# Performance work log

Measured on AMD Instinct MI355X. Metric: run time of the kernel, lower is better.

## Reference

```python
import jax, jax.numpy as jnp
import numpy as np

DIM = 1024; HEADS = 16; DHEAD = 64; HID = 2048; E = 8; TOPK = 2
B = 2; S = 1024; SCTX = 1024
SCALE = DHEAD ** -0.5
INNER = HEADS * DHEAD


def setup_inputs() -> dict:
    key = jax.random.key(0)
    ks = jax.random.split(key, 20)
    w = lambda k, shape: jax.random.normal(k, shape, dtype=jnp.float32) * 0.02
    return {
        'x': jax.random.normal(ks[0], (B, S, DIM), dtype=jnp.float32),
        'enc_output': jax.random.normal(ks[1], (B, SCTX, DIM), dtype=jnp.float32),
        'src_mask': jnp.zeros((B, SCTX), dtype=bool),
        'tgt_mask': jax.random.randint(ks[2], (B, S), 0, 2).astype(bool),
        'tgt_mask_id_bool': jax.random.randint(ks[3], (B, S), 0, 2).astype(bool),
        'ln1_g': jnp.ones((DIM,), jnp.float32), 'ln1_b': jnp.zeros((DIM,), jnp.float32),
        'ln2_g': jnp.ones((DIM,), jnp.float32), 'ln2_b': jnp.zeros((DIM,), jnp.float32),
        'ln3_g': jnp.ones((DIM,), jnp.float32), 'ln3_b': jnp.zeros((DIM,), jnp.float32),
        'sa_wq': w(ks[4], (DIM, INNER)), 'sa_wk': w(ks[5], (DIM, INNER)),
        'sa_wv': w(ks[6], (DIM, INNER)), 'sa_wo': w(ks[7], (INNER, DIM)),
        'sa_bo': jnp.zeros((DIM,), jnp.float32),
        'ca_wq': w(ks[8], (DIM, INNER)), 'ca_wk': w(ks[9], (DIM, INNER)),
        'ca_wv': w(ks[10], (DIM, INNER)), 'ca_wo': w(ks[11], (INNER, DIM)),
        'ca_bo': jnp.zeros((DIM,), jnp.float32),
        'gate_w': w(ks[12], (DIM, E)),
        'cls_w': w(ks[13], (DIM, 1)), 'cls_b': jnp.zeros((1,), jnp.float32),
        'moe_w1': w(ks[14], (E, DIM, HID)),
        'moe_w2': w(ks[15], (E, HID, DIM)),
        'moe_w3': w(ks[16], (E, DIM, HID)),
    }


def layer_norm(x, g, b, eps=1e-5):
    m = jnp.mean(x, -1, keepdims=True)
    v = jnp.mean((x - m) ** 2, -1, keepdims=True)
    return (x - m) * jax.lax.rsqrt(v + eps) * g + b


def attention(x, ctx, mask, wq, wk, wv, wo, bo):
    b, n, _ = x.shape
    m = ctx.shape[1]
    q = (x @ wq).reshape(b, n, HEADS, DHEAD)
    k = (ctx @ wk).reshape(b, m, HEADS, DHEAD)
    v = (ctx @ wv).reshape(b, m, HEADS, DHEAD)
    sim = jnp.einsum('bihd,bjhd->bhij', q, k) * SCALE  # [b,h,n,m]
    sim = jnp.where(mask[:, None, None, :], jnp.finfo(sim.dtype).min, sim)
    attn = jax.nn.softmax(sim, axis=-1)
    out = jnp.einsum('bhij,bjhd->bihd', attn, v).reshape(b, n, INNER)
    return out @ wo + bo


def moe_ffn(x, tgt_pad, tgt_mid, gate_w, w1, w2, w3, cls_w, cls_b):
    b, s, d = x.shape
    xf = x.reshape(-1, d)                                   # [N, D]
    n = xf.shape[0]
    probs = jax.nn.softmax((xf @ gate_w).astype(jnp.float32), axis=-1)  # [N, E]
    router_probs = probs.reshape(b, s, E)
    topw, sel = jax.lax.top_k(probs, TOPK)                  # [N, k]
    topw = (topw / topw.sum(-1, keepdims=True)).astype(x.dtype)
    # dense token->expert weight matrix (0 for unselected experts)
    wtok = jnp.zeros((n, E), x.dtype).at[jnp.arange(n)[:, None], sel].set(topw)
    # SwiGLU experts computed densely, masked by routing weights
    h = jax.nn.silu(jnp.einsum('nd,edh->enh', xf, w1)) * jnp.einsum('nd,edh->enh', xf, w3)
    contrib = jnp.einsum('enh,ehd->end', h, w2) * wtok.T[:, :, None]    # [E, N, D]
    cum = jnp.cumsum(contrib, axis=0)                       # state after each expert's index_add_
    final = cum[-1].reshape(b, s, d)
    keep = (~(tgt_mid | tgt_pad)).astype(x.dtype)           # [b, s], 1 = non-padding
    denom = jnp.maximum(keep.sum(1), 1.0)                   # [b]
    emb = jnp.einsum('ebsd,bs->ebd', cum.reshape(E, b, s, d), keep) / denom[None, :, None]
    logits = emb @ cls_w + cls_b                            # [E, b, 1]
    return final, logits, router_probs


def reference(x, enc_output, src_mask, tgt_mask, tgt_mask_id_bool,
              ln1_g, ln1_b, ln2_g, ln2_b, ln3_g, ln3_b,
              sa_wq, sa_wk, sa_wv, sa_wo, sa_bo,
              ca_wq, ca_wk, ca_wv, ca_wo, ca_bo,
              gate_w, cls_w, cls_b, moe_w1, moe_w2, moe_w3):
    # self attention + residual + norm1
    attn_out = attention(x, x, tgt_mask, sa_wq, sa_wk, sa_wv, sa_wo, sa_bo)
    x = layer_norm(x + attn_out, ln1_g, ln1_b)
    # cross attention with encoder output + residual + norm2
    attn_out = attention(x, enc_output, src_mask, ca_wq, ca_wk, ca_wv, ca_wo, ca_bo)
    x = layer_norm(x + attn_out, ln2_g, ln2_b)
    # MoE feed forward + residual + norm3
    ff_out, expert_logits, router_probs = moe_ffn(
        x, tgt_mask, tgt_mask_id_bool, gate_w, moe_w1, moe_w2, moe_w3, cls_w, cls_b)
    x = layer_norm(x + ff_out, ln3_g, ln3_b)
    return x, expert_logits, router_probs
```

## Files before the change

### kernel.cpp

```cpp
#include <hip/hip_runtime.h>
#include <hip/hip_bf16.h>
#include <math.h>

constexpr int kB   = 2;
constexpr int kS   = 1024;
constexpr int kD   = 1024;
constexpr int kH   = 16;
constexpr int kDH  = 64;
constexpr int kHID = 2048;
constexpr int kE   = 8;
constexpr int kTok = kB * kS;
constexpr float kScale = 0.125f;
constexpr long long kOutLogits = (long long)kTok * kD;
constexpr long long kOutProbs  = kOutLogits + kE * kB;

using u16 = unsigned short;
typedef __attribute__((ext_vector_type(8))) short short8;
typedef __attribute__((ext_vector_type(4))) float f32x4;

__device__ __forceinline__ float b2f(u16 u) {
  union { unsigned int i; float f; } c; c.i = ((unsigned int)u) << 16; return c.f;
}
__device__ __forceinline__ u16 f2b(float f) {
  __hip_bfloat16 h = __float2bfloat16(f);
  u16 u; __builtin_memcpy(&u, &h, 2); return u;
}
__device__ __forceinline__ float ldIn(const void* p, long long i, int f32) {
  return f32 ? ((const float*)p)[i] : b2f(((const u16*)p)[i]);
}
__device__ __forceinline__ void ld8f(const void* p, long long i, int f32, float v[8]) {
  if (f32) {
    const float* fp = (const float*)p + i;
    float4 a = *(const float4*)fp, b = *(const float4*)(fp + 4);
    v[0]=a.x; v[1]=a.y; v[2]=a.z; v[3]=a.w; v[4]=b.x; v[5]=b.y; v[6]=b.z; v[7]=b.w;
  } else {
    short8 s = *(const short8*)((const u16*)p + i);
#pragma unroll
    for (int j = 0; j < 8; j++) v[j] = b2f((u16)s[j]);
  }
}
__device__ __forceinline__ void stOut(void* base, long long i, float v, int f32) {
  if (f32) ((float*)base)[i] = v; else ((u16*)base)[i] = f2b(v);
}

__device__ __forceinline__ void gll16(const void* g, void* l) {
  __builtin_amdgcn_global_load_lds(
      (__attribute__((address_space(1))) unsigned int*)(unsigned long long)g,
      (__attribute__((address_space(3))) unsigned int*)l, 16, 0, 0);
}

__device__ __forceinline__ float blockReduceSum(float v) {
  __shared__ float sh[4];
  int lane = threadIdx.x & 63, wv = threadIdx.x >> 6;
#pragma unroll
  for (int o = 32; o; o >>= 1) v += __shfl_down(v, o, 64);
  __syncthreads();
  if (lane == 0) sh[wv] = v;
  __syncthreads();
  return sh[0] + sh[1] + sh[2] + sh[3];
}
__device__ __forceinline__ float blockReduceMax(float v) {
  __shared__ float sh[4];
  int lane = threadIdx.x & 63, wv = threadIdx.x >> 6;
#pragma unroll
  for (int o = 32; o; o >>= 1) v = fmaxf(v, __shfl_down(v, o, 64));
  __syncthreads();
  if (lane == 0) sh[wv] = v;
  __syncthreads();
  return fmaxf(fmaxf(sh[0], sh[1]), fmaxf(sh[2], sh[3]));
}

__global__ void detect_k(const void* x, int* dflag) {
  __shared__ int sg, st;
  int tid = threadIdx.x;
  if (tid == 0) { sg = 0; st = 0; }
  __syncthreads();
  const unsigned int* w = (const unsigned int*)x;
  int good = 0, tot = 0;
  for (int i = tid; i < 1024; i += 256) {
    unsigned int lo = w[i] & 0xffffu;
    if (lo) {
      tot++;
      unsigned int e = (lo >> 7) & 0xffu;
      if (e >= 97 && e <= 159) good++;
    }
  }
  atomicAdd(&sg, good); atomicAdd(&st, tot);
  __syncthreads();
  if (tid == 0) dflag[0] = (sg * 10 < st * 9) ? 1 : 0;
}

__global__ __launch_bounds__(256) void fattn_k(const float* Q, const float* K,
                                               const float* V, const float* maskf,
                                               float* O) {
  const int qt = blockIdx.x, bh = blockIdx.y;
  const int b = bh >> 4, hoff = (bh & 15) * 64;
  const int tid = threadIdx.x, wave = tid >> 6, lane = tid & 63;
  const int quad = lane >> 4, l16 = lane & 15, l7 = lane & 7;

  __shared__ __align__(16) u16 Ksh[64][64], Ksl[64][64];
  __shared__ __align__(16) u16 Vth[64][64], Vtl[64][64];
  __shared__ __align__(16) u16 PsArr[4][2][1024];

  const long long tok0 = (long long)b * kS;
  const long long q0 = tok0 + qt * 64;

  short8 qh[2], qlo[2];
  {
    const float* qp = Q + (q0 + wave * 16 + l16) * kD + hoff + quad * 8;
#pragma unroll
    for (int kt = 0; kt < 2; kt++) {
      float4 x0 = *(const float4*)(qp + kt * 32);
      float4 x1 = *(const float4*)(qp + kt * 32 + 4);
      float vv[8] = {x0.x, x0.y, x0.z, x0.w, x1.x, x1.y, x1.z, x1.w};
#pragma unroll
      for (int j = 0; j < 8; j++) {
        u16 hh = f2b(vv[j]);
        qh[kt][j] = (short)hh;
        qlo[kt][j] = (short)f2b(vv[j] - b2f(hh));
      }
    }
  }

  f32x4 o[4];
  const f32x4 z4 = {0.f, 0.f, 0.f, 0.f};
  o[0] = z4; o[1] = z4; o[2] = z4; o[3] = z4;
  float mrow[4] = {-3e38f, -3e38f, -3e38f, -3e38f};
  float lrow[4] = {0.f, 0.f, 0.f, 0.f};

  const int srow = tid >> 2, sd = (tid & 3) * 2;
  const int sx = srow & 7;

#pragma unroll 1
  for (int t = 0; t < 16; t++) {
    if (t) __syncthreads();
    {
      const float* kp = K + (tok0 + t * 64 + srow) * kD + hoff + sd * 8;
      float4 a0 = *(const float4*)kp, a1 = *(const float4*)(kp + 4);
      float4 a2 = *(const float4*)(kp + 8), a3 = *(const float4*)(kp + 12);
      float vv[16] = {a0.x,a0.y,a0.z,a0.w, a1.x,a1.y,a1.z,a1.w,
                      a2.x,a2.y,a2.z,a2.w, a3.x,a3.y,a3.z,a3.w};
      short8 h0, l0, h1, l1;
#pragma unroll
      for (int j = 0; j < 8; j++) {
        u16 ha = f2b(vv[j]);     h0[j] = (short)ha; l0[j] = (short)f2b(vv[j] - b2f(ha));
        u16 hb = f2b(vv[8 + j]); h1[j] = (short)hb; l1[j] = (short)f2b(vv[8 + j] - b2f(hb));
      }
      *(short8*)&Ksh[srow][(sd ^ sx) << 3] = h0;
      *(short8*)&Ksl[srow][(sd ^ sx) << 3] = l0;
      *(short8*)&Ksh[srow][((sd + 1) ^ sx) << 3] = h1;
      *(short8*)&Ksl[srow][((sd + 1) ^ sx) << 3] = l1;
    }
    {
      const float* vp = V + (tok0 + t * 64 + srow) * kD + hoff + sd * 8;
      float4 a0 = *(const float4*)vp, a1 = *(const float4*)(vp + 4);
      float4 a2 = *(const float4*)(vp + 8), a3 = *(const float4*)(vp + 12);
      float vv[16] = {a0.x,a0.y,a0.z,a0.w, a1.x,a1.y,a1.z,a1.w,
                      a2.x,a2.y,a2.z,a2.w, a3.x,a3.y,a3.z,a3.w};
      const int kvg = srow >> 3, kvo = srow & 7;
#pragma unroll
      for (int j = 0; j < 16; j++) {
        const int d = sd * 8 + j;
        const int idx = ((kvg ^ (d & 7)) << 3) + kvo;
        u16 hh = f2b(vv[j]);
        Vth[d][idx] = hh;
        Vtl[d][idx] = f2b(vv[j] - b2f(hh));
      }
    }
    __syncthreads();
    f32x4 sa[4];
    sa[0] = z4; sa[1] = z4; sa[2] = z4; sa[3] = z4;
#pragma unroll
    for (int kt = 0; kt < 2; kt++) {
      const int g = ((kt * 4 + quad) ^ l7) << 3;
#pragma unroll
      for (int n = 0; n < 4; n++) {
        short8 bh = *(const short8*)&Ksh[n * 16 + l16][g];
        short8 bl = *(const short8*)&Ksl[n * 16 + l16][g];
        sa[n] = __builtin_amdgcn_mfma_f32_16x16x32_bf16(qlo[kt], bh, sa[n], 0, 0, 0);
        sa[n] = __builtin_amdgcn_mfma_f32_16x16x32_bf16(qh[kt], bl, sa[n], 0, 0, 0);
        sa[n] = __builtin_amdgcn_mfma_f32_16x16x32_bf16(qh[kt], bh, sa[n], 0, 0, 0);
      }
    }
    float s_[4][4];
    float pm[4] = {-3e38f, -3e38f, -3e38f, -3e38f};
#pragma unroll
    for (int n = 0; n < 4; n++) {
      const bool mb = maskf[b * kS + t * 64 + n * 16 + l16] != 0.f;
#pragma unroll
      for (int r = 0; r < 4; r++) {
        float v = mb ? -1e30f : sa[n][r] * kScale;
        s_[n][r] = v;
        pm[r] = fmaxf(pm[r], v);
      }
    }
#pragma unroll
    for (int mo = 1; mo < 16; mo <<= 1) {
#pragma unroll
      for (int r = 0; r < 4; r++) pm[r] = fmaxf(pm[r], __shfl_xor(pm[r], mo, 64));
    }
    float alpha[4], rs[4];
#pragma unroll
    for (int r = 0; r < 4; r++) {
      float mn = fmaxf(mrow[r], pm[r]);
      alpha[r] = __expf(mrow[r] - mn);
      mrow[r] = mn;
      rs[r] = 0.f;
    }
#pragma unroll
    for (int n = 0; n < 4; n++) {
#pragma unroll
      for (int r = 0; r < 4; r++) {
        float p = __expf(s_[n][r] - mrow[r]);
        s_[n][r] = p;
        rs[r] += p;
      }
    }
#pragma unroll
    for (int mo = 1; mo < 16; mo <<= 1) {
#pragma unroll
      for (int r = 0; r < 4; r++) rs[r] += __shfl_xor(rs[r], mo, 64);
    }
#pragma unroll
    for (int r = 0; r < 4; r++) {
      lrow[r] = lrow[r] * alpha[r] + rs[r];
#pragma unroll
      for (int n = 0; n < 4; n++) o[n][r] *= alpha[r];
    }
#pragma unroll
    for (int n = 0; n < 4; n++) {
      const int cg = n * 2 + (l16 >> 3);
#pragma unroll
      for (int r = 0; r < 4; r++) {
        const int row = quad * 4 + r;
        const int idx = row * 64 + ((cg ^ (row & 7)) << 3) + l7;
        u16 hh = f2b(s_[n][r]);
        PsArr[wave][0][idx] = hh;
        PsArr[wave][1][idx] = f2b(s_[n][r] - b2f(hh));
      }
    }
    __syncthreads();
#pragma unroll
    for (int ks = 0; ks < 2; ks++) {
      const int g = ((ks * 4 + quad) ^ l7) << 3;
      short8 ph = *(const short8*)&PsArr[wave][0][l16 * 64 + g];
      short8 pl = *(const short8*)&PsArr[wave][1][l16 * 64 + g];
#pragma unroll
      for (int n = 0; n < 4; n++) {
        short8 vh = *(const short8*)&Vth[n * 16 + l16][g];
        short8 vl = *(const short8*)&Vtl[n * 16 + l16][g];
        o[n] = __builtin_amdgcn_mfma_f32_16x16x32_bf16(pl, vh, o[n], 0, 0, 0);
        o[n] = __builtin_amdgcn_mfma_f32_16x16x32_bf16(ph, vl, o[n], 0, 0, 0);
        o[n] = __builtin_amdgcn_mfma_f32_16x16x32_bf16(ph, vh, o[n], 0, 0, 0);
      }
    }
  }
#pragma unroll
  for (int r = 0; r < 4; r++) {
    const float inv = 1.f / lrow[r];
    float* op = O + (q0 + wave * 16 + quad * 4 + r) * kD + hoff;
#pragma unroll
    for (int n = 0; n < 4; n++) op[n * 16 + l16] = o[n][r] * inv;
  }
}

__global__ __launch_bounds__(256) void splitW_k(const void* s0, const void* s1, const void* s2,
                                                u16* h0, u16* l0, u16* h1, u16* l1,
                                                u16* h2, u16* l2, const int* dflag) {
  const int f32 = dflag[0];
  const void* src = blockIdx.z == 0 ? s0 : (blockIdx.z == 1 ? s1 : s2);
  u16* hi = blockIdx.z == 0 ? h0 : (blockIdx.z == 1 ? h1 : h2);
  u16* lo = blockIdx.z == 0 ? l0 : (blockIdx.z == 1 ? l1 : l2);
  const int gid = blockIdx.x * 256 + threadIdx.x;
  const int n = gid & 1023;
  const int kb8 = gid >> 10;
  const long long s0i = (long long)kb8 * 8 * 1024 + n;
  short8 h8, l8;
#pragma unroll
  for (int j = 0; j < 8; j++) {
    float v = ldIn(src, s0i + (long long)j * 1024, f32);
    u16 hh = f2b(v);
    h8[j] = (short)hh;
    l8[j] = (short)f2b(v - b2f(hh));
  }
  *(short8*)(hi + (long long)gid * 8) = h8;
  *(short8*)(lo + (long long)gid * 8) = l8;
}

__global__ __launch_bounds__(256) void splitA_k(const void* src, u16* hi, u16* lo,
                                                int forceF32, const int* dflag) {
  const int f32 = forceF32 ? 1 : dflag[0];
  const long long gid = (long long)blockIdx.x * 256 + threadIdx.x;
  float v[8];
  ld8f(src, gid * 8, f32, v);
  short8 h8, l8;
#pragma unroll
  for (int j = 0; j < 8; j++) {
    u16 hh = f2b(v[j]);
    h8[j] = (short)hh;
    l8[j] = (short)f2b(v[j] - b2f(hh));
  }
  *(short8*)(hi + gid * 8) = h8;
  *(short8*)(lo + gid * 8) = l8;
}

template <int NB>
__global__ __launch_bounds__(256) void gemmS_k(const u16* Ah, const u16* Al,
                                               const u16* Bh0, const u16* Bl0,
                                               const u16* Bh1, const u16* Bl1,
                                               const u16* Bh2, const u16* Bl2,
                                               float* C0, float* C1, float* C2,
                                               const void* bias, const int* dflag) {
  const int lin = blockIdx.y * gridDim.x + blockIdx.x;
  const int swz = (lin & 7) * 64 + (lin >> 3);
  const int tx = swz >> 5, ty = swz & 31;
  const int m0 = ty * 64, n0 = tx * 64;
  const int f32in = dflag[0];

  __shared__ __align__(16) u16 AhS[2][64][32], AlS[2][64][32];
  __shared__ __align__(16) u16 BhS[NB][2][4][64][8], BlS[NB][2][4][64][8];

  const int tid = threadIdx.x, wave = tid >> 6, lane = tid & 63;
  const int wr = wave >> 1, wc = wave & 1, quad = lane >> 4, l16 = lane & 15;

  const long long aOff = (long long)(m0 + (tid >> 2)) * kD + (tid & 3) * 8;
  const long long bOff = ((long long)(tid >> 6) * kD + n0 + (tid & 63)) * 8;
  const u16* pBh[3] = {Bh0, Bh1, Bh2};
  const u16* pBl[3] = {Bl0, Bl1, Bl2};
  float* pC[3] = {C0, C1, C2};

  f32x4 acc[NB][2][2];
  const f32x4 z4 = {0.f, 0.f, 0.f, 0.f};
#pragma unroll
  for (int i = 0; i < NB; i++) {
    acc[i][0][0] = z4; acc[i][0][1] = z4; acc[i][1][0] = z4; acc[i][1][1] = z4;
  }

  auto stage = [&](int buf, int kb) {
    gll16(Ah + aOff + kb * 32, (char*)&AhS[buf][0][0] + (wave << 10));
    gll16(Al + aOff + kb * 32, (char*)&AlS[buf][0][0] + (wave << 10));
    const long long bo = bOff + (long long)kb * (kD * 32);
#pragma unroll
    for (int i = 0; i < NB; i++) {
      gll16(pBh[i] + bo, (char*)&BhS[i][buf][0][0][0] + (wave << 10));
      gll16(pBl[i] + bo, (char*)&BlS[i][buf][0][0][0] + (wave << 10));
    }
  };

  stage(0, 0);
  __syncthreads();
  for (int kb = 0; kb < kD / 32; kb++) {
    const int cur = kb & 1;
    if (kb + 1 < kD / 32) stage(cur ^ 1, kb + 1);
    short8 ah0 = *(const short8*)&AhS[cur][wr * 32 + l16][quad * 8];
    short8 ah1 = *(const short8*)&AhS[cur][wr * 32 + 16 + l16][quad * 8];
    short8 al0 = *(const short8*)&AlS[cur][wr * 32 + l16][quad * 8];
    short8 al1 = *(const short8*)&AlS[cur][wr * 32 + 16 + l16][quad * 8];
#pragma unroll
    for (int i = 0; i < NB; i++) {
      short8 bh0 = *(const short8*)&BhS[i][cur][quad][wc * 32 + l16][0];
      short8 bh1 = *(const short8*)&BhS[i][cur][quad][wc * 32 + 16 + l16][0];
      short8 bl0 = *(const short8*)&BlS[i][cur][quad][wc * 32 + l16][0];
      short8 bl1 = *(const short8*)&BlS[i][cur][quad][wc * 32 + 16 + l16][0];
      acc[i][0][0] = __builtin_amdgcn_mfma_f32_16x16x32_bf16(al0, bh0, acc[i][0][0], 0, 0, 0);
      acc[i][0][1] = __builtin_amdgcn_mfma_f32_16x16x32_bf16(al0, bh1, acc[i][0][1], 0, 0, 0);
      acc[i][1][0] = __builtin_amdgcn_mfma_f32_16x16x32_bf16(al1, bh0, acc[i][1][0], 0, 0, 0);
      acc[i][1][1] = __builtin_amdgcn_mfma_f32_16x16x32_bf16(al1, bh1, acc[i][1][1], 0, 0, 0);
      acc[i][0][0] = __builtin_amdgcn_mfma_f32_16x16x32_bf16(ah0, bl0, acc[i][0][0], 0, 0, 0);
      acc[i][0][1] = __builtin_amdgcn_mfma_f32_16x16x32_bf16(ah0, bl1, acc[i][0][1], 0, 0, 0);
      acc[i][1][0] = __builtin_amdgcn_mfma_f32_16x16x32_bf16(ah1, bl0, acc[i][1][0], 0, 0, 0);
      acc[i][1][1] = __builtin_amdgcn_mfma_f32_16x16x32_bf16(ah1, bl1, acc[i][1][1], 0, 0, 0);
      acc[i][0][0] = __builtin_amdgcn_mfma_f32_16x16x32_bf16(ah0, bh0, acc[i][0][0], 0, 0, 0);
      acc[i][0][1] = __builtin_amdgcn_mfma_f32_16x16x32_bf16(ah0, bh1, acc[i][0][1], 0, 0, 0);
      acc[i][1][0] = __builtin_amdgcn_mfma_f32_16x16x32_bf16(ah1, bh0, acc[i][1][0], 0, 0, 0);
      acc[i][1][1] = __builtin_amdgcn_mfma_f32_16x16x32_bf16(ah1, bh1, acc[i][1][1], 0, 0, 0);
    }
    __syncthreads();
  }

#pragma unroll
  for (int i = 0; i < NB; i++) {
#pragma unroll
    for (int sm = 0; sm < 2; sm++) {
#pragma unroll
      for (int r = 0; r < 4; r++) {
        int row = m0 + wr * 32 + sm * 16 + quad * 4 + r;
#pragma unroll
        for (int sn = 0; sn < 2; sn++) {
          int col = n0 + wc * 32 + sn * 16 + l16;
          float v = acc[i][sm][sn][r];
          if (bias && i == 0) v += ldIn(bias, col, f32in);
          pC[i][(long long)row * kD + col] = v;
        }
      }
    }
  }
}

__global__ __launch_bounds__(256) void cvtW_k(const void* src, u16* dst,
                                              int nSh, int kbSh, const int* dflag) {
  const int f32 = dflag[0];
  const int gid = blockIdx.x * 256 + threadIdx.x;
  const int N = 1 << nSh;
  const int n = gid & (N - 1);
  const int rest = gid >> nSh;
  const int kg = rest & 3;
  const int kb = (rest >> 2) & ((1 << kbSh) - 1);
  const int e = rest >> (2 + kbSh);
  const long long src0 = ((long long)e << (5 + kbSh + nSh)) +
                         (long long)(kb * 32 + kg * 8) * N + n;
  short8 o;
#pragma unroll
  for (int j = 0; j < 8; j++) o[j] = (short)f2b(ldIn(src, src0 + (long long)j * N, f32));
  *(short8*)(dst + (long long)gid * 8) = o;
}

__global__ __launch_bounds__(256) void cvtX_k(const float* src, u16* dst) {
  const int gid = blockIdx.x * 256 + threadIdx.x;
  const float* s = src + (long long)gid * 8;
  float4 a = *(const float4*)s, b = *(const float4*)(s + 4);
  short8 o;
  o[0]=(short)f2b(a.x); o[1]=(short)f2b(a.y); o[2]=(short)f2b(a.z); o[3]=(short)f2b(a.w);
  o[4]=(short)f2b(b.x); o[5]=(short)f2b(b.y); o[6]=(short)f2b(b.z); o[7]=(short)f2b(b.w);
  *(short8*)(dst + (long long)gid * 8) = o;
}

__global__ __launch_bounds__(256) void moe13_k(const u16* Xb, const u16* W1c, const u16* W3c,
                                               const int* counts, const int* offsets,
                                               const int* aidxArr, u16* Hbuf) {
  const int e = blockIdx.z;
  const int Meff = counts[e];
  const int m0 = blockIdx.y * 64;
  if (m0 >= Meff) return;
  const int n0 = blockIdx.x * 128;
  const int csr = offsets[e];

  __shared__ __align__(16) u16 As[2][64][32];
  __shared__ __align__(16) u16 B1s[2][4][128][8];
  __shared__ __align__(16) u16 B3s[2][4][128][8];

  const int tid = threadIdx.x, wave = tid >> 6, lane = tid & 63;
  const int wc = wave, quad = lane >> 4, l16 = lane & 15;

  int grow = m0 + (tid >> 2); if (grow >= Meff) grow = Meff - 1;
  const u16* pA = Xb + (long long)aidxArr[csr + grow] * kD + (tid & 3) * 8;

  const long long ebase = (long long)e * kD * kHID;
  const int g0 = tid, g1 = 256 + tid;
  const long long b0o = ebase + ((long long)(g0 >> 7) * kHID + n0 + (g0 & 127)) * 8;
  const long long b1o = ebase + ((long long)(g1 >> 7) * kHID + n0 + (g1 & 127)) * 8;

  f32x4 acc1[4][2], acc3[4][2];
  const f32x4 z4 = {0.f, 0.f, 0.f, 0.f};
#pragma unroll
  for (int i = 0; i < 4; i++) { acc1[i][0]=z4; acc1[i][1]=z4; acc3[i][0]=z4; acc3[i][1]=z4; }

  auto stage = [&](int buf, int kb) {
    gll16(pA + kb * 32, (char*)&As[buf][0][0] + (wave << 10));
    const long long ko = (long long)kb * (4 * kHID * 8);
    gll16(W1c + b0o + ko, (char*)&B1s[buf][0][0][0] + (wave << 10));
    gll16(W1c + b1o + ko, (char*)&B1s[buf][0][0][0] + 4096 + (wave << 10));
    gll16(W3c + b0o + ko, (char*)&B3s[buf][0][0][0] + (wave << 10));
    gll16(W3c + b1o + ko, (char*)&B3s[buf][0][0][0] + 4096 + (wave << 10));
  };

  stage(0, 0);
  __syncthreads();
  for (int kb = 0; kb < kD / 32; kb++) {
    const int cur = kb & 1;
    if (kb + 1 < kD / 32) stage(cur ^ 1, kb + 1);
    short8 af[4];
#pragma unroll
    for (int sm = 0; sm < 4; sm++)
      af[sm] = *(const short8*)&As[cur][sm * 16 + l16][quad * 8];
    short8 b1f[2], b3f[2];
#pragma unroll
    for (int sn = 0; sn < 2; sn++) {
      b1f[sn] = *(const short8*)&B1s[cur][quad][wc * 32 + sn * 16 + l16][0];
      b3f[sn] = *(const short8*)&B3s[cur][quad][wc * 32 + sn * 16 + l16][0];
    }
#pragma unroll
    for (int sm = 0; sm < 4; sm++) {
#pragma unroll
      for (int sn = 0; sn < 2; sn++) {
        acc1[sm][sn] = __builtin_amdgcn_mfma_f32_16x16x32_bf16(af[sm], b1f[sn], acc1[sm][sn], 0, 0, 0);
        acc3[sm][sn] = __builtin_amdgcn_mfma_f32_16x16x32_bf16(af[sm], b3f[sn], acc3[sm][sn], 0, 0, 0);
      }
    }
    __syncthreads();
  }

#pragma unroll
  for (int sm = 0; sm < 4; sm++) {
#pragma unroll
    for (int r = 0; r < 4; r++) {
      int row = m0 + sm * 16 + quad * 4 + r;
      if (row >= Meff) continue;
#pragma unroll
      for (int sn = 0; sn < 2; sn++) {
        int col = n0 + wc * 32 + sn * 16 + l16;
        float g1 = acc1[sm][sn][r], g3 = acc3[sm][sn][r];
        float h = (g1 / (1.f + __expf(-g1))) * g3;
        Hbuf[(long long)(csr + row) * kHID + col] = f2b(h);
      }
    }
  }
}

__global__ __launch_bounds__(256) void w2_k(const u16* Hbuf, const u16* W2c,
                                            const int* counts, const int* offsets,
                                            const int* aidxArr, const int* slotArr,
                                            const float* wgtArr, float* contrib) {
  const int e = blockIdx.z;
  const int Meff = counts[e];
  const int m0 = blockIdx.y * 64;
  if (m0 >= Meff) return;
  const int n0 = blockIdx.x * 128;
  const int csr = offsets[e];

  __shared__ __align__(16) u16 As[2][64][32];
  __shared__ __align__(16) u16 Bs[2][4][128][8];

  const int tid = threadIdx.x, wave = tid >> 6, lane = tid & 63;
  const int wc = wave, quad = lane >> 4, l16 = lane & 15;

  int grow = m0 + (tid >> 2); if (grow >= Meff) grow = Meff - 1;
  const u16* pA = Hbuf + (long long)(csr + grow) * kHID + (tid & 3) * 8;

  const long long ebase = (long long)e * kHID * kD;
  const int g0 = tid, g1 = 256 + tid;
  const long long b0o = ebase + ((long long)(g0 >> 7) * kD + n0 + (g0 & 127)) * 8;
  const long long b1o = ebase + ((long long)(g1 >> 7) * kD + n0 + (g1 & 127)) * 8;

  f32x4 acc[4][2];
  const f32x4 z4 = {0.f, 0.f, 0.f, 0.f};
#pragma unroll
  for (int i = 0; i < 4; i++) { acc[i][0] = z4; acc[i][1] = z4; }

  auto stage = [&](int buf, int kb) {
    gll16(pA + kb * 32, (char*)&As[buf][0][0] + (wave << 10));
    const long long ko = (long long)kb * (4 * kD * 8);
    gll16(W2c + b0o + ko, (char*)&Bs[buf][0][0][0] + (wave << 10));
    gll16(W2c + b1o + ko, (char*)&Bs[buf][0][0][0] + 4096 + (wave << 10));
  };

  stage(0, 0);
  __syncthreads();
  for (int kb = 0; kb < kHID / 32; kb++) {
    const int cur = kb & 1;
    if (kb + 1 < kHID / 32) stage(cur ^ 1, kb + 1);
    short8 af[4];
#pragma unroll
    for (int sm = 0; sm < 4; sm++)
      af[sm] = *(const short8*)&As[cur][sm * 16 + l16][quad * 8];
    short8 bf[2];
#pragma unroll
    for (int sn = 0; sn < 2; sn++)
      bf[sn] = *(const short8*)&Bs[cur][quad][wc * 32 + sn * 16 + l16][0];
#pragma unroll
    for (int sm = 0; sm < 4; sm++) {
#pragma unroll
      for (int sn = 0; sn < 2; sn++)
        acc[sm][sn] = __builtin_amdgcn_mfma_f32_16x16x32_bf16(af[sm], bf[sn], acc[sm][sn], 0, 0, 0);
    }
    __syncthreads();
  }

#pragma unroll
  for (int sm = 0; sm < 4; sm++) {
#pragma unroll
    for (int r = 0; r < 4; r++) {
      int row = m0 + sm * 16 + quad * 4 + r;
      if (row >= Meff) continue;
      int a = csr + row;
      int t = aidxArr[a]; int s = slotArr[a]; float w = wgtArr[a];
#pragma unroll
      for (int sn = 0; sn < 2; sn++) {
        int col = n0 + wc * 32 + sn * 16 + l16;
        contrib[((long long)s * kTok + t) * kD + col] = acc[sm][sn][r] * w;
      }
    }
  }
}

__global__ void maskprep_k(const void* srcm, const void* tgtm, const void* midm,
                           float* srcf, float* padf, float* keepf, float* denom) {
  __shared__ int okInt, okFloat, okBf16;
  int tid = threadIdx.x;
  if (tid == 0) { okInt = 1; okFloat = 1; okBf16 = 1; }
  __syncthreads();
  const unsigned int* wi = (const unsigned int*)tgtm;
  const float* wf = (const float*)tgtm;
  int badI = 0, badF = 0, badB = 0;
  for (int i = tid; i < 512; i += 256) {
    unsigned int w = wi[i];
    if (w > 1u) badI = 1;
    float f = wf[i];
    if (!(f == 0.f || f == 1.f)) badF = 1;
    unsigned int lo = w & 0xffffu, hi = w >> 16;
    if (!((lo == 0 || lo == 0x3f80u) && (hi == 0 || hi == 0x3f80u))) badB = 1;
  }
  if (badI) atomicExch(&okInt, 0);
  if (badF) atomicExch(&okFloat, 0);
  if (badB) atomicExch(&okBf16, 0);
  __syncthreads();
  int mode = okInt ? 0 : (okFloat ? 2 : (okBf16 ? 3 : 1));
  for (int i = tid; i < kTok; i += 256) {
    bool sv, pv, mv;
    if (mode == 0) {
      sv = ((const int*)srcm)[i] != 0; pv = ((const int*)tgtm)[i] != 0; mv = ((const int*)midm)[i] != 0;
    } else if (mode == 2) {
      sv = ((const float*)srcm)[i] != 0.f; pv = ((const float*)tgtm)[i] != 0.f; mv = ((const float*)midm)[i] != 0.f;
    } else if (mode == 3) {
      sv = ((const u16*)srcm)[i] != 0; pv = ((const u16*)tgtm)[i] != 0; mv = ((const u16*)midm)[i] != 0;
    } else {
      sv = ((const unsigned char*)srcm)[i] != 0; pv = ((const unsigned char*)tgtm)[i] != 0; mv = ((const unsigned char*)midm)[i] != 0;
    }
    srcf[i] = sv ? 1.f : 0.f;
    padf[i] = pv ? 1.f : 0.f;
    keepf[i] = (pv || mv) ? 0.f : 1.f;
  }
  __syncthreads();
  if (tid < 2) {
    float s = 0;
    for (int j = 0; j < kS; j++) s += keepf[tid * kS + j];
    denom[tid] = fmaxf(s, 1.f);
  }
}

__global__ __launch_bounds__(256) void ln_k(const float* basef, const void* baseb,
                                            const int* dflag, int baseIsIn,
                                            const float* add1, const float* add2,
                                            const void* g, const void* bb,
                                            float* outf, void* outFinal) {
  const int f32in = dflag[0];
  const int baseF32 = baseIsIn && f32in;
  long long base = (long long)blockIdx.x * kD;
  int tid = threadIdx.x;
  float v[4]; float s = 0;
#pragma unroll
  for (int i = 0; i < 4; i++) {
    int d = tid + i * 256;
    float x = basef ? basef[base + d] : ldIn(baseb, base + d, baseF32);
    if (add1) x += add1[base + d];
    if (add2) x += add2[base + d];
    v[i] = x; s += x;
  }
  float mean = blockReduceSum(s) * (1.f / kD);
  float q = 0;
#pragma unroll
  for (int i = 0; i < 4; i++) { float d0 = v[i] - mean; q += d0 * d0; }
  float var = blockReduceSum(q) * (1.f / kD);
  float rstd = rsqrtf(var + 1e-5f);
#pragma unroll
  for (int i = 0; i < 4; i++) {
    int d = tid + i * 256;
    float y = (v[i] - mean) * rstd * ldIn(g, d, f32in) + ldIn(bb, d, f32in);
    if (outf) outf[base + d] = y;
    if (outFinal) stOut(outFinal, base + d, y, f32in);
  }
}

__global__ __launch_bounds__(256) void router_k(const float* xf, const void* gw, void* outBase,
                                                int* sel, float* wsel, int* counts,
                                                const int* dflag) {
  const int f32in = dflag[0];
  int wv = threadIdx.x >> 6, lane = threadIdx.x & 63;
  int t = blockIdx.x * 4 + wv;
  const float* xr = xf + (long long)t * kD;
  float acc[8];
#pragma unroll
  for (int e = 0; e < 8; e++) acc[e] = 0.f;
  for (int d = lane; d < kD; d += 64) {
    float xv = xr[d];
    float gv[8];
    ld8f(gw, (long long)d * 8, f32in, gv);
#pragma unroll
    for (int e = 0; e < 8; e++) acc[e] += xv * gv[e];
  }
#pragma unroll
  for (int o = 32; o; o >>= 1) {
#pragma unroll
    for (int e = 0; e < 8; e++) acc[e] += __shfl_down(acc[e], o, 64);
  }
  if (lane == 0) {
    float mx = acc[0];
    for (int e = 1; e < 8; e++) mx = fmaxf(mx, acc[e]);
    float p[8], sum = 0;
    for (int e = 0; e < 8; e++) { p[e] = expf(acc[e] - mx); sum += p[e]; }
    float inv = 1.f / sum;
    for (int e = 0; e < 8; e++) {
      p[e] *= inv;
      stOut(outBase, kOutProbs + (long long)t * 8 + e, p[e], f32in);
    }
    int e0 = 0; for (int e = 1; e < 8; e++) if (p[e] > p[e0]) e0 = e;
    int e1 = -1; for (int e = 0; e < 8; e++) { if (e == e0) continue; if (e1 < 0 || p[e] > p[e1]) e1 = e; }
    float s2 = p[e0] + p[e1];
    sel[t * 2] = e0; sel[t * 2 + 1] = e1;
    wsel[t * 2] = p[e0] / s2; wsel[t * 2 + 1] = p[e1] / s2;
    atomicAdd(&counts[e0], 1); atomicAdd(&counts[e1], 1);
  }
}

__global__ void offsets_k(const int* counts, int* offsets) {
  if (threadIdx.x == 0) {
    int s = 0;
    for (int e = 0; e < kE; e++) { offsets[e] = s; s += counts[e]; }
    offsets[kE] = s;
  }
}

__global__ void place_k(const int* sel, const float* wsel, const int* offsets, int* fill,
                        int* aidxArr, int* slotArr, float* wgtArr) {
  int t = blockIdx.x * 256 + threadIdx.x;
  if (t >= kTok) return;
  for (int s = 0; s < 2; s++) {
    int e = sel[t * 2 + s];
    int pos = offsets[e] + atomicAdd(&fill[e], 1);
    aidxArr[pos] = t; slotArr[pos] = s; wgtArr[pos] = wsel[t * 2 + s];
  }
}

__global__ void meanacc_k(const int* counts, const int* offsets, const int* aidxArr,
                          const int* slotArr, const float* keepf, const float* contrib,
                          float* meanAcc) {
  int e = blockIdx.x, dc = blockIdx.y, ch = blockIdx.z;
  int d = dc * 128 + threadIdx.x;
  int cnt = counts[e], off = offsets[e];
  int per = (cnt + 15) / 16;
  int i0 = ch * per, i1 = i0 + per; if (i1 > cnt) i1 = cnt;
  float a0 = 0, a1 = 0;
  for (int i = i0; i < i1; i++) {
    int a = off + i; int t = aidxArr[a];
    if (keepf[t] != 0.f) {
      float v = contrib[((long long)slotArr[a] * kTok + t) * kD + d];
      if (t < kS) a0 += v; else a1 += v;
    }
  }
  if (a0 != 0.f) atomicAdd(&meanAcc[(e * 2 + 0) * kD + d], a0);
  if (a1 != 0.f) atomicAdd(&meanAcc[(e * 2 + 1) * kD + d], a1);
}

__global__ __launch_bounds__(256) void dots_k(const float* meanAcc, const void* cls_w,
                                              const float* denom, float* dots,
                                              const int* dflag) {
  const int f32in = dflag[0];
  int eb = blockIdx.x;
  int b = eb & 1;
  float s = 0;
  for (int d = threadIdx.x; d < kD; d += 256)
    s += meanAcc[(long long)eb * kD + d] * ldIn(cls_w, d, f32in);
  s = blockReduceSum(s);
  if (threadIdx.x == 0) dots[eb] = s / denom[b];
}

__global__ void final_logits_k(const float* dots, const void* cls_b, void* outBase,
                               const int* dflag) {
  const int f32in = dflag[0];
  int i = threadIdx.x;
  if (i < kE * kB) {
    int e = i >> 1, b = i & 1;
    float s = ldIn(cls_b, 0, f32in);
    for (int e2 = 0; e2 <= e; e2++) s += dots[e2 * 2 + b];
    stOut(outBase, kOutLogits + e * kB + b, s, f32in);
  }
}

extern "C" void kernel_launch(void* const* d_in, const int* in_sizes, int n_in,
                              void* d_out, int out_size, void* d_ws, size_t ws_size,
                              hipStream_t stream) {
  (void)in_sizes; (void)n_in; (void)out_size; (void)ws_size;

  const void* x_in  = d_in[0];
  const void* enc   = d_in[1];
  const void* srcm = d_in[2];
  const void* tgtm = d_in[3];
  const void* midm = d_in[4];
  const void* ln1g = d_in[5];  const void* ln1b = d_in[6];
  const void* ln2g = d_in[7];  const void* ln2b = d_in[8];
  const void* ln3g = d_in[9];  const void* ln3b = d_in[10];
  const void* sa_wq = d_in[11]; const void* sa_wk = d_in[12];
  const void* sa_wv = d_in[13]; const void* sa_wo = d_in[14];
  const void* sa_bo = d_in[15];
  const void* ca_wq = d_in[16]; const void* ca_wk = d_in[17];
  const void* ca_wv = d_in[18]; const void* ca_wo = d_in[19];
  const void* ca_bo = d_in[20];
  const void* gate_w = d_in[21];
  const void* cls_w  = d_in[22]; const void* cls_b = d_in[23];
  const void* moe_w1 = d_in[24];
  const void* moe_w2 = d_in[25];
  const void* moe_w3 = d_in[26];

  char* wp = (char*)d_ws;
  size_t off = 0;
  auto alloc = [&](size_t bytes) -> void* {
    void* p = wp + off; off = (off + bytes + 255) & ~(size_t)255; return p;
  };
  float* scFP = (float*)alloc((size_t)16 * kS * kS * 4);
  u16*   Hbuf = (u16*)scFP;
  float* contrib = (float*)((char*)scFP + (size_t)2 * kTok * kHID * 2);
  float* qf    = (float*)alloc((size_t)kTok * kD * 4);
  float* kf    = (float*)alloc((size_t)kTok * kD * 4);
  float* vf    = (float*)alloc((size_t)kTok * kD * 4);
  float* attnof= (float*)alloc((size_t)kTok * kD * 4);
  float* obuf  = (float*)alloc((size_t)kTok * kD * 4);
  float* x1f   = (float*)alloc((size_t)kTok * kD * 4);
  float* x2f   = (float*)alloc((size_t)kTok * kD * 4);
  float* meanAcc = (float*)alloc((size_t)kE * kB * kD * 4);
  float* srcf = (float*)alloc(kTok * 4);
  float* padf = (float*)alloc(kTok * 4);
  float* keepf = (float*)alloc(kTok * 4);
  float* denom = (float*)alloc(2 * 4);
  int* counts = (int*)alloc(256); int* fill = counts + 8;
  int* offsets = (int*)alloc(256);
  int* sel = (int*)alloc(kTok * 2 * 4);
  float* wsel = (float*)alloc(kTok * 2 * 4);
  int* aidxArr = (int*)alloc(2 * kTok * 4);
  int* slotArr = (int*)alloc(2 * kTok * 4);
  float* wgtArr = (float*)alloc(2 * kTok * 4);
  float* dots = (float*)alloc(256);
  int* dflag = (int*)alloc(256);

  u16* WH0 = (u16*)x2f;
  u16* WL0 = WH0 + (1 << 20);
  u16* WH1 = WL0 + (1 << 20);
  u16* WL1 = WH1 + (1 << 20);
  u16* WH2 = (u16*)x1f;
  u16* WL2 = WH2 + (1 << 20);
  u16* AH  = (u16*)scFP;
  u16* AL  = AH + (2 << 20);

  u16* W1c = (u16*)qf;
  u16* W2c = (u16*)qf;
  u16* W3c = (u16*)((char*)scFP + ((size_t)32 << 20));
  u16* Xb  = (u16*)obuf;

  hipMemsetAsync(counts, 0, 64, stream);
  hipMemsetAsync(meanAcc, 0, (size_t)kE * kB * kD * 4, stream);
  detect_k<<<1, 256, 0, stream>>>(x_in, dflag);
  maskprep_k<<<1, 256, 0, stream>>>(srcm, tgtm, midm, srcf, padf, keepf, denom);

  const dim3 gGrid(16, 32);
  const dim3 aGrid(kS / 64, 32);

  splitA_k<<<1024, 256, 0, stream>>>(x_in, AH, AL, 0, dflag);
  splitW_k<<<dim3(512, 1, 3), 256, 0, stream>>>(sa_wq, sa_wk, sa_wv,
      WH0, WL0, WH1, WL1, WH2, WL2, dflag);
  gemmS_k<3><<<gGrid, 256, 0, stream>>>(AH, AL, WH0, WL0, WH1, WL1, WH2, WL2,
      qf, kf, vf, nullptr, dflag);
  fattn_k<<<aGrid, 256, 0, stream>>>(qf, kf, vf, padf, attnof);
  splitA_k<<<1024, 256, 0, stream>>>(attnof, AH, AL, 1, dflag);
  splitW_k<<<dim3(512, 1, 1), 256, 0, stream>>>(sa_wo, nullptr, nullptr,
      WH0, WL0, nullptr, nullptr, nullptr, nullptr, dflag);
  gemmS_k<1><<<gGrid, 256, 0, stream>>>(AH, AL, WH0, WL0, WH0, WL0, WH0, WL0,
      obuf, obuf, obuf, sa_bo, dflag);
  ln_k<<<kTok, 256, 0, stream>>>(nullptr, x_in, dflag, 1, obuf, nullptr, ln1g, ln1b, x1f, nullptr);

  splitA_k<<<1024, 256, 0, stream>>>(x1f, AH, AL, 1, dflag);
  splitW_k<<<dim3(512, 1, 1), 256, 0, stream>>>(ca_wq, nullptr, nullptr,
      WH0, WL0, nullptr, nullptr, nullptr, nullptr, dflag);
  gemmS_k<1><<<gGrid, 256, 0, stream>>>(AH, AL, WH0, WL0, WH0, WL0, WH0, WL0,
      qf, qf, qf, nullptr, dflag);
  splitA_k<<<1024, 256, 0, stream>>>(enc, AH, AL, 0, dflag);
  splitW_k<<<dim3(512, 1, 2), 256, 0, stream>>>(ca_wk, ca_wv, nullptr,
      WH0, WL0, WH1, WL1, nullptr, nullptr, dflag);
  gemmS_k<2><<<gGrid, 256, 0, stream>>>(AH, AL, WH0, WL0, WH1, WL1, WH0, WL0,
      kf, vf, vf, nullptr, dflag);
  fattn_k<<<aGrid, 256, 0, stream>>>(qf, kf, vf, srcf, attnof);
  splitA_k<<<1024, 256, 0, stream>>>(attnof, AH, AL, 1, dflag);
  splitW_k<<<dim3(512, 1, 1), 256, 0, stream>>>(ca_wo, nullptr, nullptr,
      WH0, WL0, nullptr, nullptr, nullptr, nullptr, dflag);
  gemmS_k<1><<<gGrid, 256, 0, stream>>>(AH, AL, WH0, WL0, WH0, WL0, WH0, WL0,
      obuf, obuf, obuf, ca_bo, dflag);
  ln_k<<<kTok, 256, 0, stream>>>(x1f, nullptr, dflag, 0, obuf, nullptr, ln2g, ln2b, x2f, nullptr);

  router_k<<<kTok / 4, 256, 0, stream>>>(x2f, gate_w, d_out, sel, wsel, counts, dflag);
  offsets_k<<<1, 64, 0, stream>>>(counts, offsets);
  place_k<<<kTok / 256, 256, 0, stream>>>(sel, wsel, offsets, fill, aidxArr, slotArr, wgtArr);

  cvtX_k<<<kTok * kD / (8 * 256), 256, 0, stream>>>(x2f, Xb);
  const int wGrid = (kE * kD * kHID / 8) / 256;
  cvtW_k<<<wGrid, 256, 0, stream>>>(moe_w1, W1c, 11, 5, dflag);
  cvtW_k<<<wGrid, 256, 0, stream>>>(moe_w3, W3c, 11, 5, dflag);

  moe13_k<<<dim3(kHID / 128, kTok / 64, kE), 256, 0, stream>>>(
      Xb, W1c, W3c, counts, offsets, aidxArr, Hbuf);

  cvtW_k<<<wGrid, 256, 0, stream>>>(moe_w2, W2c, 10, 6, dflag);

  w2_k<<<dim3(kD / 128, kTok / 64, kE), 256, 0, stream>>>(
      Hbuf, W2c, counts, offsets, aidxArr, slotArr, wgtArr, contrib);

  meanacc_k<<<dim3(kE, kD / 128, 16), 128, 0, stream>>>(counts, offsets, aidxArr, slotArr, keepf, contrib, meanAcc);
  dots_k<<<kE * kB, 256, 0, stream>>>(meanAcc, cls_w, denom, dots, dflag);
  final_logits_k<<<1, 64, 0, stream>>>(dots, cls_b, d_out, dflag);
  ln_k<<<kTok, 256, 0, stream>>>(x2f, nullptr, dflag, 0, contrib, contrib + (size_t)kTok * kD, ln3g, ln3b, nullptr, d_out);
}
```

Before: 931.4 us.

## Emit split bf16 hi/lo from GEMMs and consume them directly in flash attention

The Q/K/V projection GEMMs now write their outputs as bf16 hi/lo pairs instead of fp32. The attention kernel loads those pairs directly and writes its output as hi/lo pairs, which lets two splitA passes over the attention output be dropped and removes per-tile conversion inside attention. K/V tiles are also prefetched into registers for the next iteration, overlapping global loads with compute, and the LDS swizzle key changes. Memory traffic per element stays about the same (two u16 vs one fp32), but fewer kernels and conversions run, at the cost of more register pressure from the prefetch buffers.

```diff
diff --git a/kernel.cpp b/kernel.cpp
--- a/kernel.cpp
+++ b/kernel.cpp
@@ -90,9 +90,13 @@
   if (tid == 0) dflag[0] = (sg * 10 < st * 9) ? 1 : 0;
 }
 
-__global__ __launch_bounds__(256) void fattn_k(const float* Q, const float* K,
-                                               const float* V, const float* maskf,
-                                               float* O) {
+__device__ __forceinline__ int key8(int r) { return (r ^ (r >> 3)) & 7; }
+
+__global__ __launch_bounds__(256) void fattn_k(const u16* Qh, const u16* Ql,
+                                               const u16* Kh, const u16* Kl,
+                                               const u16* Vh, const u16* Vl,
+                                               const float* maskf,
+                                               u16* Oh, u16* Ol) {
   const int qt = blockIdx.x, bh = blockIdx.y;
   const int b = bh >> 4, hoff = (bh & 15) * 64;
   const int tid = threadIdx.x, wave = tid >> 6, lane = tid & 63;
@@ -100,27 +104,26 @@
 
   __shared__ __align__(16) u16 Ksh[64][64], Ksl[64][64];
   __shared__ __align__(16) u16 Vth[64][64], Vtl[64][64];
-  __shared__ __align__(16) u16 PsArr[4][2][1024];
+  __shared__ __align__(16) u16 Ps[4][2][1024];
 
   const long long tok0 = (long long)b * kS;
   const long long q0 = tok0 + qt * 64;
 
   short8 qh[2], qlo[2];
   {
-    const float* qp = Q + (q0 + wave * 16 + l16) * kD + hoff + quad * 8;
+    const long long qoff = (q0 + wave * 16 + l16) * kD + hoff;
 #pragma unroll
     for (int kt = 0; kt < 2; kt++) {
-      float4 x0 = *(const float4*)(qp + kt * 32);
-      float4 x1 = *(const float4*)(qp + kt * 32 + 4);
-      float vv[8] = {x0.x, x0.y, x0.z, x0.w, x1.x, x1.y, x1.z, x1.w};
-#pragma unroll
-      for (int j = 0; j < 8; j++) {
-        u16 hh = f2b(vv[j]);
-        qh[kt][j] = (short)hh;
-        qlo[kt][j] = (short)f2b(vv[j] - b2f(hh));
-      }
-    }
-  }
+      qh[kt]  = *(const short8*)(Qh + qoff + kt * 32 + quad * 8);
+      qlo[kt] = *(const short8*)(Ql + qoff + kt * 32 + quad * 8);
+    }
+  }
+
+  const int g0i = tid, g1i = 256 + tid;
+  const int kr0 = g0i >> 3, kc0 = (g0i & 7) ^ key8(g0i >> 3);
+  const int kr1 = g1i >> 3, kc1 = (g1i & 7) ^ key8(g1i >> 3);
+  const int srow = tid >> 2, sd = (tid & 3) * 2;
+  const int kvg = srow >> 3, kvo = srow & 7;
 
   f32x4 o[4];
   const f32x4 z4 = {0.f, 0.f, 0.f, 0.f};
@@ -128,55 +131,51 @@
   float mrow[4] = {-3e38f, -3e38f, -3e38f, -3e38f};
   float lrow[4] = {0.f, 0.f, 0.f, 0.f};
 
-  const int srow = tid >> 2, sd = (tid & 3) * 2;
-  const int sx = srow & 7;
+  short8 pk0, pk1, pk2, pk3;
+  short8 pv0, pv1, pv2, pv3;
+
+  auto loadRegs = [&](int t) {
+    const long long kb0 = (tok0 + t * 64 + kr0) * kD + hoff + kc0 * 8;
+    const long long kb1 = (tok0 + t * 64 + kr1) * kD + hoff + kc1 * 8;
+    pk0 = *(const short8*)(Kh + kb0);
+    pk1 = *(const short8*)(Kh + kb1);
+    pk2 = *(const short8*)(Kl + kb0);
+    pk3 = *(const short8*)(Kl + kb1);
+    const long long vb = (tok0 + t * 64 + srow) * kD + hoff + sd * 8;
+    pv0 = *(const short8*)(Vh + vb);
+    pv1 = *(const short8*)(Vh + vb + 8);
+    pv2 = *(const short8*)(Vl + vb);
+    pv3 = *(const short8*)(Vl + vb + 8);
+  };
+
+  loadRegs(0);
 
 #pragma unroll 1
   for (int t = 0; t < 16; t++) {
     if (t) __syncthreads();
-    {
-      const float* kp = K + (tok0 + t * 64 + srow) * kD + hoff + sd * 8;
-      float4 a0 = *(const float4*)kp, a1 = *(const float4*)(kp + 4);
-      float4 a2 = *(const float4*)(kp + 8), a3 = *(const float4*)(kp + 12);
-      float vv[16] = {a0.x,a0.y,a0.z,a0.w, a1.x,a1.y,a1.z,a1.w,
-                      a2.x,a2.y,a2.z,a2.w, a3.x,a3.y,a3.z,a3.w};
-      short8 h0, l0, h1, l1;
-#pragma unroll
-      for (int j = 0; j < 8; j++) {
-        u16 ha = f2b(vv[j]);     h0[j] = (short)ha; l0[j] = (short)f2b(vv[j] - b2f(ha));
-        u16 hb = f2b(vv[8 + j]); h1[j] = (short)hb; l1[j] = (short)f2b(vv[8 + j] - b2f(hb));
-      }
-      *(short8*)&Ksh[srow][(sd ^ sx) << 3] = h0;
-      *(short8*)&Ksl[srow][(sd ^ sx) << 3] = l0;
-      *(short8*)&Ksh[srow][((sd + 1) ^ sx) << 3] = h1;
-      *(short8*)&Ksl[srow][((sd + 1) ^ sx) << 3] = l1;
-    }
-    {
-      const float* vp = V + (tok0 + t * 64 + srow) * kD + hoff + sd * 8;
-      float4 a0 = *(const float4*)vp, a1 = *(const float4*)(vp + 4);
-      float4 a2 = *(const float4*)(vp + 8), a3 = *(const float4*)(vp + 12);
-      float vv[16] = {a0.x,a0.y,a0.z,a0.w, a1.x,a1.y,a1.z,a1.w,
-                      a2.x,a2.y,a2.z,a2.w, a3.x,a3.y,a3.z,a3.w};
-      const int kvg = srow >> 3, kvo = srow & 7;
-#pragma unroll
-      for (int j = 0; j < 16; j++) {
-        const int d = sd * 8 + j;
-        const int idx = ((kvg ^ (d & 7)) << 3) + kvo;
-        u16 hh = f2b(vv[j]);
-        Vth[d][idx] = hh;
-        Vtl[d][idx] = f2b(vv[j] - b2f(hh));
-      }
+    *(short8*)((u16*)Ksh + g0i * 8) = pk0;
+    *(short8*)((u16*)Ksh + g1i * 8) = pk1;
+    *(short8*)((u16*)Ksl + g0i * 8) = pk2;
+    *(short8*)((u16*)Ksl + g1i * 8) = pk3;
+#pragma unroll
+    for (int j = 0; j < 16; j++) {
+      const int d = sd * 8 + j;
+      const int idx = ((kvg ^ key8(d)) << 3) + kvo;
+      Vth[d][idx] = (u16)(j < 8 ? pv0[j] : pv1[j - 8]);
+      Vtl[d][idx] = (u16)(j < 8 ? pv2[j] : pv3[j - 8]);
     }
     __syncthreads();
+    if (t + 1 < 16) loadRegs(t + 1);
     f32x4 sa[4];
     sa[0] = z4; sa[1] = z4; sa[2] = z4; sa[3] = z4;
 #pragma unroll
     for (int kt = 0; kt < 2; kt++) {
-      const int g = ((kt * 4 + quad) ^ l7) << 3;
 #pragma unroll
       for (int n = 0; n < 4; n++) {
-        short8 bh = *(const short8*)&Ksh[n * 16 + l16][g];
-        short8 bl = *(const short8*)&Ksl[n * 16 + l16][g];
+        const int row = n * 16 + l16;
+        const int g = (((kt * 4 + quad) ^ key8(row)) << 3);
+        short8 bh = *(const short8*)&Ksh[row][g];
+        short8 bl = *(const short8*)&Ksl[row][g];
         sa[n] = __builtin_amdgcn_mfma_f32_16x16x32_bf16(qlo[kt], bh, sa[n], 0, 0, 0);
         sa[n] = __builtin_amdgcn_mfma_f32_16x16x32_bf16(qh[kt], bl, sa[n], 0, 0, 0);
         sa[n] = __builtin_amdgcn_mfma_f32_16x16x32_bf16(qh[kt], bh, sa[n], 0, 0, 0);
@@ -233,22 +232,24 @@
 #pragma unroll
       for (int r = 0; r < 4; r++) {
         const int row = quad * 4 + r;
-        const int idx = row * 64 + ((cg ^ (row & 7)) << 3) + l7;
+        const int idx = row * 64 + ((cg ^ key8(row)) << 3) + l7;
         u16 hh = f2b(s_[n][r]);
-        PsArr[wave][0][idx] = hh;
-        PsArr[wave][1][idx] = f2b(s_[n][r] - b2f(hh));
+        Ps[wave][0][idx] = hh;
+        Ps[wave][1][idx] = f2b(s_[n][r] - b2f(hh));
       }
     }
     __syncthreads();
 #pragma unroll
     for (int ks = 0; ks < 2; ks++) {
-      const int g = ((ks * 4 + quad) ^ l7) << 3;
-      short8 ph = *(const short8*)&PsArr[wave][0][l16 * 64 + g];
-      short8 pl = *(const short8*)&PsArr[wave][1][l16 * 64 + g];
+      const int gp = (((ks * 4 + quad) ^ key8(l16)) << 3);
+      short8 ph = *(const short8*)&Ps[wave][0][l16 * 64 + gp];
+      short8 pl = *(const short8*)&Ps[wave][1][l16 * 64 + gp];
 #pragma unroll
       for (int n = 0; n < 4; n++) {
-        short8 vh = *(const short8*)&Vth[n * 16 + l16][g];
-        short8 vl = *(const short8*)&Vtl[n * 16 + l16][g];
+        const int row = n * 16 + l16;
+        const int g = (((ks * 4 + quad) ^ key8(row)) << 3);
+        short8 vh = *(const short8*)&Vth[row][g];
+        short8 vl = *(const short8*)&Vtl[row][g];
         o[n] = __builtin_amdgcn_mfma_f32_16x16x32_bf16(pl, vh, o[n], 0, 0, 0);
         o[n] = __builtin_amdgcn_mfma_f32_16x16x32_bf16(ph, vl, o[n], 0, 0, 0);
         o[n] = __builtin_amdgcn_mfma_f32_16x16x32_bf16(ph, vh, o[n], 0, 0, 0);
@@ -258,9 +259,14 @@
 #pragma unroll
   for (int r = 0; r < 4; r++) {
     const float inv = 1.f / lrow[r];
-    float* op = O + (q0 + wave * 16 + quad * 4 + r) * kD + hoff;
-#pragma unroll
-    for (int n = 0; n < 4; n++) op[n * 16 + l16] = o[n][r] * inv;
+    const long long ob = (q0 + wave * 16 + quad * 4 + r) * kD + hoff;
+#pragma unroll
+    for (int n = 0; n < 4; n++) {
+      float val = o[n][r] * inv;
+      u16 hh = f2b(val);
+      Oh[ob + n * 16 + l16] = hh;
+      Ol[ob + n * 16 + l16] = f2b(val - b2f(hh));
+    }
   }
 }
 
@@ -304,12 +310,13 @@
   *(short8*)(lo + gid * 8) = l8;
 }
 
-template <int NB>
+template <int NB, int OS>
 __global__ __launch_bounds__(256) void gemmS_k(const u16* Ah, const u16* Al,
                                                const u16* Bh0, const u16* Bl0,
                                                const u16* Bh1, const u16* Bl1,
                                                const u16* Bh2, const u16* Bl2,
-                                               float* C0, float* C1, float* C2,
+                                               void* C0, void* C1, void* C2,
+                                               u16* Cl0, u16* Cl1, u16* Cl2,
                                                const void* bias, const int* dflag) {
   const int lin = blockIdx.y * gridDim.x + blockIdx.x;
   const int swz = (lin & 7) * 64 + (lin >> 3);
@@ -327,7 +334,8 @@
   const long long bOff = ((long long)(tid >> 6) * kD + n0 + (tid & 63)) * 8;
   const u16* pBh[3] = {Bh0, Bh1, Bh2};
   const u16* pBl[3] = {Bl0, Bl1, Bl2};
-  float* pC[3] = {C0, C1, C2};
+  void* pC[3] = {C0, C1, C2};
+  u16* pCl[3] = {Cl0, Cl1, Cl2};
 
   f32x4 acc[NB][2][2];
   const f32x4 z4 = {0.f, 0.f, 0.f, 0.f};
@@ -389,8 +397,15 @@
         for (int sn = 0; sn < 2; sn++) {
           int col = n0 + wc * 32 + sn * 16 + l16;
           float v = acc[i][sm][sn][r];
-          if (bias && i == 0) v += ldIn(bias, col, f32in);
-          pC[i][(long long)row * kD + col] = v;
+          const long long idx = (long long)row * kD + col;
+          if (OS) {
+            u16 hh = f2b(v);
+            ((u16*)pC[i])[idx] = hh;
+            pCl[i][idx] = f2b(v - b2f(hh));
+          } else {
+            if (bias && i == 0) v += ldIn(bias, col, f32in);
+            ((float*)pC[i])[idx] = v;
+          }
         }
       }
     }
@@ -830,6 +845,11 @@
   u16* AH  = (u16*)scFP;
   u16* AL  = AH + (2 << 20);
 
+  u16* Qh = (u16*)qf;     u16* Ql = Qh + (2 << 20);
+  u16* Kh = (u16*)kf;     u16* Kl = Kh + (2 << 20);
+  u16* Vh = (u16*)vf;     u16* Vl = Vh + (2 << 20);
+  u16* Oh = (u16*)attnof; u16* Ol = Oh + (2 << 20);
+
   u16* W1c = (u16*)qf;
   u16* W2c = (u16*)qf;
   u16* W3c = (u16*)((char*)scFP + ((size_t)32 << 20));
@@ -846,32 +866,30 @@
   splitA_k<<<1024, 256, 0, stream>>>(x_in, AH, AL, 0, dflag);
   splitW_k<<<dim3(512, 1, 3), 256, 0, stream>>>(sa_wq, sa_wk, sa_wv,
       WH0, WL0, WH1, WL1, WH2, WL2, dflag);
-  gemmS_k<3><<<gGrid, 256, 0, stream>>>(AH, AL, WH0, WL0, WH1, WL1, WH2, WL2,
-      qf, kf, vf, nullptr, dflag);
-  fattn_k<<<aGrid, 256, 0, stream>>>(qf, kf, vf, padf, attnof);
-  splitA_k<<<1024, 256, 0, stream>>>(attnof, AH, AL, 1, dflag);
+  gemmS_k<3, 1><<<gGrid, 256, 0, stream>>>(AH, AL, WH0, WL0, WH1, WL1, WH2, WL2,
+      Qh, Kh, Vh, Ql, Kl, Vl, nullptr, dflag);
+  fattn_k<<<aGrid, 256, 0, stream>>>(Qh, Ql, Kh, Kl, Vh, Vl, padf, Oh, Ol);
   splitW_k<<<dim3(512, 1, 1), 256, 0, stream>>>(sa_wo, nullptr, nullptr,
       WH0, WL0, nullptr, nullptr, nullptr, nullptr, dflag);
-  gemmS_k<1><<<gGrid, 256, 0, stream>>>(AH, AL, WH0, WL0, WH0, WL0, WH0, WL0,
-      obuf, obuf, obuf, sa_bo, dflag);
+  gemmS_k<1, 0><<<gGrid, 256, 0, stream>>>(Oh, Ol, WH0, WL0, WH0, WL0, WH0, WL0,
+      obuf, obuf, obuf, nullptr, nullptr, nullptr, sa_bo, dflag);
   ln_k<<<kTok, 256, 0, stream>>>(nullptr, x_in, dflag, 1, obuf, nullptr, ln1g, ln1b, x1f, nullptr);
 
   splitA_k<<<1024, 256, 0, stream>>>(x1f, AH, AL, 1, dflag);
   splitW_k<<<dim3(512, 1, 1), 256, 0, stream>>>(ca_wq, nullptr, nullptr,
       WH0, WL0, nullptr, nullptr, nullptr, nullptr, dflag);
-  gemmS_k<1><<<gGrid, 256, 0, stream>>>(AH, AL, WH0, WL0, WH0, WL0, WH0, WL0,
-      qf, qf, qf, nullptr, dflag);
+  gemmS_k<1, 1><<<gGrid, 256, 0, stream>>>(AH, AL, WH0, WL0, WH0, WL0, WH0, WL0,
+      Qh, Qh, Qh, Ql, Ql, Ql, nullptr, dflag);
   splitA_k<<<1024, 256, 0, stream>>>(enc, AH, AL, 0, dflag);
   splitW_k<<<dim3(512, 1, 2), 256, 0, stream>>>(ca_wk, ca_wv, nullptr,
       WH0, WL0, WH1, WL1, nullptr, nullptr, dflag);
-  gemmS_k<2><<<gGrid, 256, 0, stream>>>(AH, AL, WH0, WL0, WH1, WL1, WH0, WL0,
-      kf, vf, vf, nullptr, dflag);
-  fattn_k<<<aGrid, 256, 0, stream>>>(qf, kf, vf, srcf, attnof);
-  splitA_k<<<1024, 256, 0, stream>>>(attnof, AH, AL, 1, dflag);
+  gemmS_k<2, 1><<<gGrid, 256, 0, stream>>>(AH, AL, WH0, WL0, WH1, WL1, WH0, WL0,
+      Kh, Vh, Vh, Kl, Vl, Vl, nullptr, dflag);
+  fattn_k<<<aGrid, 256, 0, stream>>>(Qh, Ql, Kh, Kl, Vh, Vl, srcf, Oh, Ol);
   splitW_k<<<dim3(512, 1, 1), 256, 0, stream>>>(ca_wo, nullptr, nullptr,
       WH0, WL0, nullptr, nullptr, nullptr, nullptr, dflag);
-  gemmS_k<1><<<gGrid, 256, 0, stream>>>(AH, AL, WH0, WL0, WH0, WL0, WH0, WL0,
-      obuf, obuf, obuf, ca_bo, dflag);
+  gemmS_k<1, 0><<<gGrid, 256, 0, stream>>>(Oh, Ol, WH0, WL0, WH0, WL0, WH0, WL0,
+      obuf, obuf, obuf, nullptr, nullptr, nullptr, ca_bo, dflag);
   ln_k<<<kTok, 256, 0, stream>>>(x1f, nullptr, dflag, 0, obuf, nullptr, ln2g, ln2b, x2f, nullptr);
 
   router_k<<<kTok / 4, 256, 0, stream>>>(x2f, gate_w, d_out, sel, wsel, counts, dflag);
```

Measured after the change: 899.5 us. -3.4%, faster.
